# Kernel optimization log

Measured on AMD Instinct MI355X. Metric: run time of the kernel, lower is better.

Reference implementation:

```python
import jax, jax.numpy as jnp
import numpy as np

B, C, H, W = 64, 3, 64, 64
F = 96          # base_filters
K = 8           # n_mixtures
h, w = H // 2, W // 2
C0 = 2 * C      # channels of each checkerboard half
SECTIONS = [C0, C0, C0 * K, C0 * K, C0 * K]
SPLITS = [int(s) for s in np.cumsum(SECTIONS)[:-1]]
EPS = 1e-6


def conv2d(x, wgt, b):
    y = jax.lax.conv_general_dilated(x, wgt, (1, 1), 'SAME',
                                     dimension_numbers=('NCHW', 'OIHW', 'NCHW'))
    return y + b[None, :, None, None]


def layer_norm(x, g, b, eps=1e-5):
    # nn.LayerNorm(mid_shape): normalize over (C,H,W) per sample
    mu = jnp.mean(x, axis=(1, 2, 3), keepdims=True)
    var = jnp.var(x, axis=(1, 2, 3), keepdims=True)
    return (x - mu) / jnp.sqrt(var + eps) * g[None] + b[None]


def checker_split(z, odd=False):
    Bz, Cz, Hz, Wz = z.shape
    z = z.reshape(Bz, Cz, Hz // 2, 2, Wz // 2, 2)
    p00 = z[:, :, :, 0, :, 0]; p01 = z[:, :, :, 0, :, 1]
    p10 = z[:, :, :, 1, :, 0]; p11 = z[:, :, :, 1, :, 1]
    z0 = jnp.concatenate([p00, p11], axis=1)  # even checkerboard
    z1 = jnp.concatenate([p01, p10], axis=1)  # odd checkerboard
    if odd:
        z0, z1 = z1, z0
    return z0, z1


def checker_merge(z0, z1, odd=False):
    if odd:
        z0, z1 = z1, z0
    Cz = z0.shape[1] // 2
    p00, p11 = z0[:, :Cz], z0[:, Cz:]
    p01, p10 = z1[:, :Cz], z1[:, Cz:]
    Bz, _, hz, wz = p00.shape
    zi = jnp.stack([jnp.stack([p00, p01], axis=-1),
                    jnp.stack([p10, p11], axis=-1)], axis=-2)  # (B,C,h,w,2i,2j)
    z = zi.transpose(0, 1, 2, 4, 3, 5).reshape(Bz, Cz, 2 * hz, 2 * wz)
    return z


def gated_attn(x, qkv_w, qkv_b, proj_w, proj_b):
    Bx, Fx, hx, wx = x.shape
    xf = x.reshape(Bx, Fx, hx * wx).transpose(0, 2, 1)  # (B, L, F)
    qkv = xf @ qkv_w.T + qkv_b
    q, k, v = jnp.split(qkv, 3, axis=-1)
    scores = jnp.einsum('bqf,bkf->bqk', q, k) / jnp.sqrt(jnp.float32(Fx))
    attn = jax.nn.softmax(scores, axis=-1)
    o = jnp.einsum('bqk,bkf->bqf', attn, v)
    g = o @ proj_w.T + proj_b
    ga, gb = jnp.split(g, 2, axis=-1)
    out = xf + ga * jax.nn.sigmoid(gb)  # gated residual
    return out.transpose(0, 2, 1).reshape(Bx, Fx, hx, wx)


def conditioner(z1, conv1_w, conv1_b, gconv_w, gconv_b, ln1_g, ln1_b,
                qkv_w, qkv_b, proj_w, proj_b, ln2_g, ln2_b, conv2_w, conv2_b):
    x = conv2d(z1, conv1_w, conv1_b)
    g = conv2d(x, gconv_w, gconv_b)
    ga, gb = jnp.split(g, 2, axis=1)
    x = x + ga * jax.nn.sigmoid(gb)          # GatedConv2d
    x = layer_norm(x, ln1_g, ln1_b)
    x = gated_attn(x, qkv_w, qkv_b, proj_w, proj_b)
    x = layer_norm(x, ln2_g, ln2_b)
    return conv2d(x, conv2_w, conv2_b)


def _forward(z, log_df_dz, conv1_w, conv1_b, gconv_w, gconv_b, ln1_g, ln1_b,
             qkv_w, qkv_b, proj_w, proj_b, ln2_g, ln2_b, conv2_w, conv2_b,
             a_log_scale, a_bias):
    z0, z1 = checker_split(z)
    params = conditioner(z1, conv1_w, conv1_b, gconv_w, gconv_b, ln1_g, ln1_b,
                         qkv_w, qkv_b, proj_w, proj_b, ln2_g, ln2_b, conv2_w, conv2_b)
    a, b, logpi, mu, s = jnp.split(params, SPLITS, axis=1)
    a = jnp.tanh(a) * a_log_scale + a_bias
    Bz = z0.shape[0]
    logpi = jax.nn.log_softmax(logpi.reshape(Bz, K, C0, h, w), axis=1)
    mu = mu.reshape(Bz, K, C0, h, w)
    s = s.reshape(Bz, K, C0, h, w)
    # mixture-of-logistics CDF
    u = (z0[:, None] - mu) * jnp.exp(-s)
    x = jnp.sum(jnp.exp(logpi) * jax.nn.sigmoid(u), axis=1)
    log_pdf = jax.scipy.special.logsumexp(
        logpi - s + jax.nn.log_sigmoid(u) + jax.nn.log_sigmoid(-u), axis=1)
    log_df_dz = log_df_dz + jnp.sum(log_pdf.reshape(Bz, -1), axis=1)
    # logit transform
    x = jnp.clip(x, EPS, 1.0 - EPS)
    z0n = jnp.log(x) - jnp.log1p(-x)
    log_df_dz = log_df_dz + jnp.sum((-jnp.log(x) - jnp.log1p(-x)).reshape(Bz, -1), axis=1)
    # affine rescale
    z0n = z0n * jnp.exp(a) + b
    log_df_dz = log_df_dz + jnp.sum(a.reshape(Bz, -1), axis=1)
    return checker_merge(z0n, z1), log_df_dz


def setup_inputs() -> dict:
    key = jax.random.key(0)
    ks = jax.random.split(key, 10)
    sc = 0.05
    return dict(
        z=jax.random.normal(ks[0], (B, C, H, W), jnp.float32),
        log_df_dz=jnp.zeros((B,), jnp.float32),
        conv1_w=sc * jax.random.normal(ks[1], (F, C0, 3, 3), jnp.float32),
        conv1_b=jnp.zeros((F,), jnp.float32),
        gconv_w=sc * jax.random.normal(ks[2], (2 * F, F, 3, 3), jnp.float32),
        gconv_b=jnp.zeros((2 * F,), jnp.float32),
        ln1_g=jnp.ones((F, h, w), jnp.float32),
        ln1_b=jnp.zeros((F, h, w), jnp.float32),
        qkv_w=sc * jax.random.normal(ks[3], (3 * F, F), jnp.float32),
        qkv_b=jnp.zeros((3 * F,), jnp.float32),
        proj_w=sc * jax.random.normal(ks[4], (2 * F, F), jnp.float32),
        proj_b=jnp.zeros((2 * F,), jnp.float32),
        ln2_g=jnp.ones((F, h, w), jnp.float32),
        ln2_b=jnp.zeros((F, h, w), jnp.float32),
        conv2_w=sc * jax.random.normal(ks[5], (sum(SECTIONS), F, 3, 3), jnp.float32),
        conv2_b=jnp.zeros((sum(SECTIONS),), jnp.float32),
        a_log_scale=0.01 * jax.random.normal(ks[6], (1,), jnp.float32),
        a_bias=0.01 * jax.random.normal(ks[7], (1,), jnp.float32),
    )


def reference(z, log_df_dz, conv1_w, conv1_b, gconv_w, gconv_b, ln1_g, ln1_b,
              qkv_w, qkv_b, proj_w, proj_b, ln2_g, ln2_b, conv2_w, conv2_b,
              a_log_scale, a_bias):
    return _forward(z, log_df_dz, conv1_w, conv1_b, gconv_w, gconv_b, ln1_g, ln1_b,
                    qkv_w, qkv_b, proj_w, proj_b, ln2_g, ln2_b, conv2_w, conv2_b,
                    a_log_scale, a_bias)
```

## Files before the change

### kernel.cpp

```cpp
#include <hip/hip_runtime.h>
#include <cstdint>
#include <cstddef>


typedef unsigned short u16;
typedef __attribute__((ext_vector_type(8))) short short8;
typedef __attribute__((ext_vector_type(4))) float f32x4;
typedef __attribute__((ext_vector_type(4))) unsigned int u32x4;

__device__ __forceinline__ float sigm(float x){ return 1.0f/(1.0f+__expf(-x)); }

__device__ __forceinline__ u16 f2bf(float f){
    unsigned int u = __float_as_uint(f);
    u += 0x7fffu + ((u >> 16) & 1u);
    return (u16)(u >> 16);
}
__device__ __forceinline__ float bf2f(u16 v){
    unsigned int u = ((unsigned int)v) << 16;
    return __uint_as_float(u);
}

__device__ __forceinline__ void dma16(const u16* g, u16* l){
    __builtin_amdgcn_global_load_lds(
        (const __attribute__((address_space(1))) void*)g,
        (__attribute__((address_space(3))) void*)l,
        16, 0, 0);
}

__device__ __forceinline__ float ex2(float x){
    float r; asm("v_exp_f32 %0, %1" : "=v"(r) : "v"(x)); return r;
}
__device__ __forceinline__ unsigned cvtpk(float lo, float hi){
    unsigned r; asm("v_cvt_pk_bf16_f32 %0, %1, %2" : "=v"(r) : "v"(lo), "v"(hi)); return r;
}
__device__ __forceinline__ void plswap32(unsigned &a, unsigned &b){
    asm("v_permlane32_swap_b32 %0, %1" : "+v"(a), "+v"(b));
}
__device__ __forceinline__ void plswap16(unsigned &a, unsigned &b){
    asm("v_permlane16_swap_b32 %0, %1" : "+v"(a), "+v"(b));
}

#define SOFTPACK(S, LACC, PA) do { \
    unsigned pk_[4][2]; \
    _Pragma("unroll") \
    for (int t=0;t<4;++t){ \
        float e0 = ex2(S[t][0]); \
        float e1 = ex2(S[t][1]); \
        float e2 = ex2(S[t][2]); \
        float e3 = ex2(S[t][3]); \
        LACC += (e0+e1)+(e2+e3); \
        pk_[t][0] = cvtpk(e0,e1); \
        pk_[t][1] = cvtpk(e2,e3); \
    } \
    _Pragma("unroll") \
    for (int kk=0;kk<2;++kk){ \
        unsigned a0 = pk_[2*kk][0], b0 = pk_[2*kk+1][0]; \
        unsigned a1 = pk_[2*kk][1], b1 = pk_[2*kk+1][1]; \
        plswap32(a0,b0); plswap16(a0,b0); \
        plswap32(a1,b1); plswap16(a1,b1); \
        u32x4 dw_; dw_[0]=a0; dw_[1]=a1; dw_[2]=b0; dw_[3]=b1; \
        PA[kk] = __builtin_bit_cast(short8, dw_); \
    } \
} while(0)

__device__ __forceinline__ short8 ln_frag(const u16* __restrict__ xg,
    const float* __restrict__ gt, const float* __restrict__ bt,
    int p, int c0, float mu, float rr)
{
    short8 x8 = *reinterpret_cast<const short8*>(xg + (size_t)p*96 + c0);
    const float* gp = gt + (size_t)p*96 + c0;
    const float* bp = bt + (size_t)p*96 + c0;
    short8 o;
    #pragma unroll
    for (int j=0;j<8;++j){
        float ag = rr*gp[j];
        o[j] = (short)f2bf(bf2f((u16)x8[j])*ag + (bp[j] - mu*ag));
    }
    return o;
}

__global__ __launch_bounds__(256) void k_prep(
    const float* __restrict__ z, const float* __restrict__ c1w, const float* __restrict__ c1b,
    const float* __restrict__ gw, const float* __restrict__ c2w,
    const float* __restrict__ qkvw, const float* __restrict__ pw,
    const float* __restrict__ ln1g, const float* __restrict__ ln1b,
    const float* __restrict__ ln2g, const float* __restrict__ ln2b,
    const float* __restrict__ logdf,
    u16* __restrict__ x1b,
    u16* __restrict__ Wg, u16* __restrict__ W2,
    u16* __restrict__ Wqkv, u16* __restrict__ Wproj,
    float* __restrict__ gt1, float* __restrict__ bt1,
    float* __restrict__ gt2, float* __restrict__ bt2,
    float* __restrict__ outlog)
{
    int blk = blockIdx.x;
    int tid = threadIdx.x;
    __shared__ float tin[6][6][34];
    __shared__ __align__(16) u16 Wc[96][72];
    __shared__ __align__(16) u16 imc[128][72];

    if (blk < 512){
        int b  = blk >> 3;
        int pg = blk & 7;
        int r0 = pg*4;
        for (int e = tid; e < 96*72; e += 256){
            int oc = e/72, k = e%72;
            Wc[oc][k] = (k < 54) ? f2bf(c1w[oc*54 + k]) : (u16)0;
        }
        for (int idx = tid; idx < 6*6*34; idx += 256){
            int c = idx/204, rem = idx%204;
            int rr = rem/34, q = rem%34;
            int ii = r0 - 1 + rr, jj = q - 1;
            float v = 0.f;
            if ((unsigned)ii < 32u && (unsigned)jj < 32u){
                if (c < 3) v = z[((b*3+c)*64 + 2*ii)*64 + (2*jj+1)];
                else       v = z[((b*3+(c-3))*64 + (2*ii+1))*64 + 2*jj];
            }
            tin[c][rr][q] = v;
        }
        __syncthreads();
        for (int e = tid; e < 128*72; e += 256){
            int px = e/72, k = e%72;
            float v = 0.f;
            if (k < 54){
                int c = k/9, rr = (k%9)/3, dcc = k%3;
                v = tin[c][(px>>5)+rr][(px&31)+dcc];
            }
            imc[px][k] = f2bf(v);
        }
        __syncthreads();

        int w = tid >> 6, lane = tid & 63;
        int cc = lane & 15, gg = lane >> 4;
        f32x4 acc[2][6];
        #pragma unroll
        for (int u=0;u<2;++u)
            #pragma unroll
            for (int t=0;t<6;++t) acc[u][t] = (f32x4){0.f,0.f,0.f,0.f};

        #pragma unroll
        for (int ks=0; ks<2; ++ks){
            short8 a0 = *reinterpret_cast<const short8*>(&imc[w*32 + cc     ][ks*32 + 8*gg]);
            short8 a1 = *reinterpret_cast<const short8*>(&imc[w*32 + 16 + cc][ks*32 + 8*gg]);
            #pragma unroll
            for (int t=0; t<6; ++t){
                short8 bb = *reinterpret_cast<const short8*>(&Wc[t*16+cc][ks*32 + 8*gg]);
                acc[0][t] = __builtin_amdgcn_mfma_f32_16x16x32_bf16(a0, bb, acc[0][t], 0,0,0);
                acc[1][t] = __builtin_amdgcn_mfma_f32_16x16x32_bf16(a1, bb, acc[1][t], 0,0,0);
            }
        }

        #pragma unroll
        for (int u=0;u<2;++u){
            int p0 = pg*128 + w*32 + u*16 + gg*4;
            #pragma unroll
            for (int t=0;t<6;++t){
                int oc = t*16+cc;
                float bv = c1b[oc];
                #pragma unroll
                for (int r=0;r<4;++r)
                    x1b[((size_t)(b*1024) + p0 + r)*96 + oc] = f2bf(acc[u][t][r] + bv);
            }
        }
    } else if (blk < 1160){
        int idx = (blk-512)*256 + tid;
        int j = idx & 7;
        int lane = (idx >> 3) & 63;
        int fo = idx >> 9;
        int frag = fo % 18;
        int tob = fo / 18;
        int obk = tob & 1, tap = tob >> 1;
        int t = frag/3, ks = frag%3;
        int cc = lane & 15, gg = lane >> 4;
        int ocp = obk*96 + t*16 + cc;
        int r2 = ocp%96, isB = r2/48, i2 = r2%48;
        int oc = (ocp/96)*48 + i2 + isB*96;
        int ic = ks*32 + 8*gg + j;
        Wg[idx] = f2bf(gw[(size_t)(oc*96+ic)*9 + tap]);
    } else if (blk < 1700){
        int idx = (blk-1160)*256 + tid;
        int j = idx & 7;
        int lane = (idx >> 3) & 63;
        int fo = idx >> 9;
        int frag = fo % 15;
        int tob = fo / 15;
        int obk = tob & 1, tap = tob >> 1;
        int t = frag/3, ks = frag%3;
        int cc = lane & 15, gg = lane >> 4;
        int oc = obk*80 + t*16 + cc;
        int ic = ks*32 + 8*gg + j;
        W2[idx] = (oc < 156) ? f2bf(c2w[(size_t)(oc*96+ic)*9 + tap]) : (u16)0;
    } else if (blk < 1808){
        int idx = (blk-1700)*256 + tid;
        int j = idx & 7;
        int lane = (idx >> 3) & 63;
        int fo = idx >> 9;
        int frag = fo % 27;
        int obk = fo / 27;
        int t = frag/3, ks = frag%3;
        int cc = lane & 15, gg = lane >> 4;
        int n = obk*144 + t*16 + cc;
        int ic = ks*32 + 8*gg + j;
        Wqkv[idx] = f2bf(qkvw[(size_t)n*96 + ic]);
    } else if (blk < 1880){
        int idx = (blk-1808)*256 + tid;
        int j = idx & 7;
        int lane = (idx >> 3) & 63;
        int fo = idx >> 9;
        int frag = fo % 18;
        int obk = fo / 18;
        int t = frag/3, ks = frag%3;
        int cc = lane & 15, gg = lane >> 4;
        int ocp = obk*96 + t*16 + cc;
        int r2 = ocp%96, isB = r2/48, i2 = r2%48;
        int oc = obk*48 + i2 + isB*96;
        int ic = ks*32 + 8*gg + j;
        Wproj[idx] = f2bf(pw[(size_t)oc*96 + ic]);
    } else if (blk < 2264){
        int idx = (blk-1880)*256 + tid;
        int c = idx >> 10, p = idx & 1023;
        gt1[p*96 + c] = ln1g[idx];
    } else if (blk < 2648){
        int idx = (blk-2264)*256 + tid;
        int c = idx >> 10, p = idx & 1023;
        bt1[p*96 + c] = ln1b[idx];
    } else if (blk < 3032){
        int idx = (blk-2648)*256 + tid;
        int c = idx >> 10, p = idx & 1023;
        gt2[p*96 + c] = ln2g[idx];
    } else if (blk < 3416){
        int idx = (blk-3032)*256 + tid;
        int c = idx >> 10, p = idx & 1023;
        bt2[p*96 + c] = ln2b[idx];
    } else {
        if (tid < 64) outlog[tid] = logdf[tid];
    }
}

__global__ __launch_bounds__(256,4) void k_gconv(const u16* __restrict__ Xpb,
    const u16* __restrict__ Wt, const float* __restrict__ bias,
    u16* __restrict__ outb, float* __restrict__ partials)
{
    int blk  = blockIdx.x;
    int obk  = blk & 1;
    int pblk = (blk >> 1) & 7;
    int b    = blk >> 4;
    int tid  = threadIdx.x;
    int w = tid >> 6, lane = tid & 63;
    int cc = lane & 15, gg = lane >> 4;

    __shared__ __align__(16) u16 Ws[2][9216];
    __shared__ float red[8];

    f32x4 acc[2][6];
    #pragma unroll
    for (int u=0;u<2;++u)
        #pragma unroll
        for (int t=0;t<6;++t) acc[u][t] = (f32x4){0.f,0.f,0.f,0.f};

    int base = pblk*128 + w*32;
    int ia = base >> 5;
    const u16* xb = Xpb + (size_t)b*1024*96;

    {
        const u16* src = Wt + (size_t)obk*9216;
        #pragma unroll
        for (int i=0;i<5;++i){
            int c = tid + 256*i;
            if (c < 1152) dma16(src + (size_t)c*8, Ws[0] + (size_t)(w*64+256*i)*8);
        }
    }

    for (int tap=0; tap<9; ++tap){
        __syncthreads();
        if (tap < 8){
            const u16* src = Wt + (size_t)((tap+1)*2 + obk)*9216;
            int nb = (tap+1)&1;
            #pragma unroll
            for (int i=0;i<5;++i){
                int c = tid + 256*i;
                if (c < 1152) dma16(src + (size_t)c*8, Ws[nb] + (size_t)(w*64+256*i)*8);
            }
        }
        const u16* Wc = Ws[tap&1];
        int dr = tap/3 - 1, dc = tap%3 - 1;

        int ii = ia + dr;
        int jj0 = cc + dc, jj1 = cc + 16 + dc;
        bool rv = ((unsigned)ii < 32u);
        bool v0 = rv && ((unsigned)jj0 < 32u);
        bool v1 = rv && ((unsigned)jj1 < 32u);
        const u16* ar0 = xb + (ptrdiff_t)(ii*32 + jj0)*96 + 8*gg;
        const u16* ar1 = xb + (ptrdiff_t)(ii*32 + jj1)*96 + 8*gg;

        #pragma unroll
        for (int ks=0; ks<3; ++ks){
            short8 a0 = {0,0,0,0,0,0,0,0};
            short8 a1 = {0,0,0,0,0,0,0,0};
            if (v0) a0 = *reinterpret_cast<const short8*>(ar0 + ks*32);
            if (v1) a1 = *reinterpret_cast<const short8*>(ar1 + ks*32);
            #pragma unroll
            for (int t=0; t<6; ++t){
                short8 bb = *reinterpret_cast<const short8*>(Wc + ((size_t)(t*3+ks)*64 + lane)*8);
                acc[0][t] = __builtin_amdgcn_mfma_f32_16x16x32_bf16(a0, bb, acc[0][t], 0,0,0);
                acc[1][t] = __builtin_amdgcn_mfma_f32_16x16x32_bf16(a1, bb, acc[1][t], 0,0,0);
            }
        }
    }

    float s = 0.f, ssq = 0.f;
    #pragma unroll
    for (int u=0;u<2;++u){
        int p0 = base + u*16 + gg*4;
        #pragma unroll
        for (int t=0;t<3;++t){
            int ocA = obk*48 + t*16+cc;
            float ba = bias[ocA], bbv = bias[ocA+96];
            #pragma unroll
            for (int r=0;r<4;++r){
                float res = bf2f(Xpb[((size_t)b*1024 + p0+r)*96 + ocA]);
                float va = acc[u][t][r]   + ba;
                float vb = acc[u][t+3][r] + bbv;
                float v = res + va*sigm(vb);
                outb[((size_t)b*1024 + p0+r)*96 + ocA] = f2bf(v);
                s += v; ssq += v*v;
            }
        }
    }
    #pragma unroll
    for (int o=32;o>0;o>>=1){ s += __shfl_down(s,o,64); ssq += __shfl_down(ssq,o,64); }
    if (lane==0){ red[w]=s; red[4+w]=ssq; }
    __syncthreads();
    if (tid==0){
        int slot = b*16 + pblk*2 + obk;
        partials[slot*2+0] = red[0]+red[1]+red[2]+red[3];
        partials[slot*2+1] = red[4]+red[5]+red[6]+red[7];
    }
}

__global__ __launch_bounds__(256) void k_lne(const u16* __restrict__ xb,
    const float* __restrict__ gt, const float* __restrict__ bt,
    const float* __restrict__ partials, u16* __restrict__ out)
{
    int b = blockIdx.x / 48, rem = blockIdx.x % 48;
    float s=0.f, ss=0.f;
    #pragma unroll
    for (int i=0;i<16;++i){ s += partials[(b*16+i)*2]; ss += partials[(b*16+i)*2+1]; }
    float mu = s/98304.f;
    float r = rsqrtf(ss/98304.f - mu*mu + 1e-5f);

    int e8 = rem*256 + threadIdx.x;
    size_t base = (size_t)b*98304 + (size_t)e8*8;
    short8 x8 = *reinterpret_cast<const short8*>(xb + base);
    const float* gp = gt + e8*8;
    const float* bp = bt + e8*8;
    short8 o8;
    #pragma unroll
    for (int i=0;i<8;++i)
        o8[i] = (short)f2bf((bf2f((u16)x8[i]) - mu)*r*gp[i] + bp[i]);
    *reinterpret_cast<short8*>(out + base) = o8;
}

__global__ __launch_bounds__(256,4) void k_qkvm(const u16* __restrict__ Xg,
    const float* __restrict__ gt, const float* __restrict__ bt,
    const float* __restrict__ part,
    const u16* __restrict__ Wt, const float* __restrict__ bias,
    u16* __restrict__ Qb, u16* __restrict__ Kf, u16* __restrict__ Vf)
{
    int blk  = blockIdx.x;
    int obk  = blk & 1;
    int pblk = (blk >> 1) & 7;
    int b    = blk >> 4;
    int tid  = threadIdx.x;
    int w = tid >> 6, lane = tid & 63;
    int cc = lane & 15, gg = lane >> 4;
    const float scale = 0.14724445f;

    __shared__ __align__(16) u16 Ws[13824];
    {
        const u16* src = Wt + (size_t)obk*13824;
        #pragma unroll
        for (int i=0;i<7;++i){
            int c = tid + 256*i;
            if (c < 1728) dma16(src + (size_t)c*8, Ws + (size_t)(w*64+256*i)*8);
        }
    }

    float sS=0.f, sQ=0.f;
    #pragma unroll
    for (int i=0;i<16;++i){ sS += part[(b*16+i)*2]; sQ += part[(b*16+i)*2+1]; }
    float mu = sS/98304.f;
    float rr = rsqrtf(sQ/98304.f - mu*mu + 1e-5f);

    f32x4 acc[2][9];
    #pragma unroll
    for (int u=0;u<2;++u)
        #pragma unroll
        for (int t=0;t<9;++t) acc[u][t] = (f32x4){0.f,0.f,0.f,0.f};

    int base = pblk*128 + w*32;
    const u16* xg = Xg + (size_t)b*1024*96;
    __syncthreads();

    #pragma unroll
    for (int ks=0; ks<3; ++ks){
        int c0 = ks*32 + 8*gg;
        short8 a0 = ln_frag(xg, gt, bt, base+cc,    c0, mu, rr);
        short8 a1 = ln_frag(xg, gt, bt, base+cc+16, c0, mu, rr);
        #pragma unroll
        for (int t=0; t<9; ++t){
            short8 bb = *reinterpret_cast<const short8*>(Ws + ((size_t)(t*3+ks)*64 + lane)*8);
            acc[0][t] = __builtin_amdgcn_mfma_f32_16x16x32_bf16(a0, bb, acc[0][t], 0,0,0);
            acc[1][t] = __builtin_amdgcn_mfma_f32_16x16x32_bf16(a1, bb, acc[1][t], 0,0,0);
        }
    }

    #pragma unroll
    for (int u=0;u<2;++u){
        int p0 = base + u*16 + gg*4;
        #pragma unroll
        for (int t=0;t<9;++t){
            int n = obk*144 + t*16+cc;
            float bv = bias[n];
            #pragma unroll
            for (int r=0;r<4;++r){
                int p = p0 + r;
                float av = acc[u][t][r] + bv;
                if (n < 96){
                    Qb[((size_t)(b*1024+p))*96 + n] = f2bf(av*scale);
                } else if (n < 192){
                    int f = n-96;
                    int jt = p>>6, t16 = (p>>4)&3, ccs = p&15;
                    int ks = f>>5, ggs = (f>>3)&3, j = f&7;
                    Kf[(size_t)(b*16+jt)*6144 + (size_t)(((t16*3+ks)*4+ggs)*16+ccs)*8 + j] = f2bf(av);
                } else {
                    int f = n-192;
                    int jt = p>>6, kl = p&63;
                    int kk = kl>>5, ggs = (kl>>3)&3, j = kl&7;
                    int ft = f>>4, ccs = f&15;
                    Vf[(size_t)(b*16+jt)*6144 + (size_t)(((ft*2+kk)*4+ggs)*16+ccs)*8 + j] = f2bf(av);
                }
            }
        }
    }
}

__global__ __launch_bounds__(256,2) void k_attnproj(const u16* __restrict__ Qb,
    const u16* __restrict__ Kf, const u16* __restrict__ Vf,
    const u16* __restrict__ Wpg, const float* __restrict__ pbias,
    const u16* __restrict__ Xg, const float* __restrict__ gt, const float* __restrict__ bt,
    const float* __restrict__ part1,
    u16* __restrict__ outb, float* __restrict__ partials)
{
    int qt = blockIdx.x >> 6;
    int b  = blockIdx.x & 63;
    int tid = threadIdx.x;
    int w  = tid >> 6;
    int lane = tid & 63;
    int cc = lane & 15;
    int gg = lane >> 4;

    __shared__ __align__(16) u16 SM[36864];
    __shared__ float red[16];

    u16* Ksb = SM;
    u16* Vsb = SM + 18432;
    u16* Wp  = SM;
    u16* Ot  = SM + 18432;

    float sS=0.f, sQ=0.f;
    #pragma unroll
    for (int i=0;i<16;++i){ sS += part1[(b*16+i)*2]; sQ += part1[(b*16+i)*2+1]; }
    float mu1 = sS/98304.f;
    float rr1 = rsqrtf(sQ/98304.f - mu1*mu1 + 1e-5f);

    int q0 = qt*128 + w*32;

    short8 qf[2][3];
    {
        const u16* qr0 = Qb + ((size_t)(b*1024 + q0 + cc))*96;
        #pragma unroll
        for (int ks=0; ks<3; ++ks){
            qf[0][ks] = *reinterpret_cast<const short8*>(qr0 + ks*32 + 8*gg);
            qf[1][ks] = *reinterpret_cast<const short8*>(qr0 + (size_t)16*96 + ks*32 + 8*gg);
        }
    }

    f32x4 Oacc[2][6];
    #pragma unroll
    for (int u=0;u<2;++u)
        #pragma unroll
        for (int ft=0; ft<6; ++ft) Oacc[u][ft] = (f32x4){0.f,0.f,0.f,0.f};
    float l_acc[2] = {0.f, 0.f};

    const u16* Kb0 = Kf + (size_t)(b*16)*6144;
    const u16* Vb0 = Vf + (size_t)(b*16)*6144;

    #pragma unroll
    for (int i=0;i<3;++i){
        size_t c8 = (size_t)(tid + 256*i)*8;
        size_t l8 = (size_t)(w*64 + 256*i)*8;
        dma16(Kb0 + c8, Ksb + l8);
        dma16(Vb0 + c8, Vsb + l8);
    }
    #pragma unroll
    for (int i=0;i<3;++i){
        size_t c8 = (size_t)(6144 + (tid + 256*i)*8);
        size_t l8 = (size_t)(w*64 + 256*i)*8;
        dma16(Kb0 + c8, Ksb + 6144 + l8);
        dma16(Vb0 + c8, Vsb + 6144 + l8);
    }

    for (int jt=0; jt<16; ++jt){
        if (jt < 15) asm volatile("s_waitcnt vmcnt(6)" ::: "memory");
        else         asm volatile("s_waitcnt vmcnt(0)" ::: "memory");
        __builtin_amdgcn_s_barrier();
        __builtin_amdgcn_sched_barrier(0);

        if (jt < 14){
            const u16* kn = Kb0 + (size_t)(jt+2)*6144;
            const u16* vn = Vb0 + (size_t)(jt+2)*6144;
            u16* kd = Ksb + (size_t)((jt+2)%3)*6144;
            u16* vd = Vsb + (size_t)((jt+2)%3)*6144;
            #pragma unroll
            for (int i=0;i<3;++i){
                size_t c8 = (size_t)(tid + 256*i)*8;
                size_t l8 = (size_t)(w*64 + 256*i)*8;
                dma16(kn + c8, kd + l8);
                dma16(vn + c8, vd + l8);
            }
        }

        const u16* Kc = Ksb + (size_t)(jt%3)*6144;
        const u16* Vc = Vsb + (size_t)(jt%3)*6144;

        f32x4 S0[4], S1[4];
        #pragma unroll
        for (int t=0;t<4;++t){ S0[t] = (f32x4){0.f,0.f,0.f,0.f}; S1[t] = (f32x4){0.f,0.f,0.f,0.f}; }

        __builtin_amdgcn_s_setprio(1);
        #pragma unroll
        for (int ks=0; ks<3; ++ks){
            #pragma unroll
            for (int t=0; t<4; ++t){
                short8 kb = *reinterpret_cast<const short8*>(Kc + ((t*3+ks)*64 + lane)*8);
                S0[t] = __builtin_amdgcn_mfma_f32_16x16x32_bf16(kb, qf[0][ks], S0[t], 0,0,0);
                S1[t] = __builtin_amdgcn_mfma_f32_16x16x32_bf16(kb, qf[1][ks], S1[t], 0,0,0);
            }
        }
        __builtin_amdgcn_s_setprio(0);

        short8 pa0[2], pa1[2];
        SOFTPACK(S0, l_acc[0], pa0);
        SOFTPACK(S1, l_acc[1], pa1);

        __builtin_amdgcn_s_setprio(1);
        #pragma unroll
        for (int kk=0; kk<2; ++kk){
            #pragma unroll
            for (int ft=0; ft<6; ++ft){
                short8 vb = *reinterpret_cast<const short8*>(Vc + ((ft*2+kk)*64 + lane)*8);
                Oacc[0][ft] = __builtin_amdgcn_mfma_f32_16x16x32_bf16(pa0[kk], vb, Oacc[0][ft], 0,0,0);
                Oacc[1][ft] = __builtin_amdgcn_mfma_f32_16x16x32_bf16(pa1[kk], vb, Oacc[1][ft], 0,0,0);
            }
        }
        __builtin_amdgcn_s_setprio(0);
    }

    __syncthreads();

    #pragma unroll
    for (int i=0;i<9;++i){
        int c = tid + 256*i;
        dma16(Wpg + (size_t)c*8, Wp + (size_t)(w*64+256*i)*8);
    }

    #pragma unroll
    for (int u=0;u<2;++u){
        float lv = l_acc[u];
        lv += __shfl_xor(lv, 16, 64);
        lv += __shfl_xor(lv, 32, 64);
        float linv[4];
        #pragma unroll
        for (int r=0;r<4;++r) linv[r] = 1.0f / __shfl(lv, 4*gg + r, 64);
        #pragma unroll
        for (int ft=0; ft<6; ++ft)
            #pragma unroll
            for (int r=0; r<4; ++r)
                Ot[(size_t)(w*32 + u*16 + 4*gg + r)*104 + ft*16 + cc]
                    = f2bf(Oacc[u][ft][r]*linv[r]);
    }

    __syncthreads();

    f32x4 pacc[2][12];
    #pragma unroll
    for (int u=0;u<2;++u)
        #pragma unroll
        for (int t=0;t<12;++t) pacc[u][t] = (f32x4){0.f,0.f,0.f,0.f};

    #pragma unroll
    for (int ks=0; ks<3; ++ks){
        short8 a0 = *reinterpret_cast<const short8*>(Ot + (size_t)(w*32 + cc     )*104 + ks*32 + 8*gg);
        short8 a1 = *reinterpret_cast<const short8*>(Ot + (size_t)(w*32 + cc + 16)*104 + ks*32 + 8*gg);
        #pragma unroll
        for (int t2=0; t2<12; ++t2){
            int obk = t2/6, tl = t2%6;
            short8 bb = *reinterpret_cast<const short8*>(Wp + ((size_t)(obk*18 + tl*3 + ks)*64 + lane)*8);
            pacc[0][t2] = __builtin_amdgcn_mfma_f32_16x16x32_bf16(a0, bb, pacc[0][t2], 0,0,0);
            pacc[1][t2] = __builtin_amdgcn_mfma_f32_16x16x32_bf16(a1, bb, pacc[1][t2], 0,0,0);
        }
    }

    const u16* resb = Xg + (size_t)b*1024*96;
    float s0=0.f, q0s=0.f, s1=0.f, q1s=0.f;
    #pragma unroll
    for (int u=0;u<2;++u){
        int p0 = qt*128 + w*32 + u*16 + gg*4;
        #pragma unroll
        for (int obk=0;obk<2;++obk){
            #pragma unroll
            for (int tl=0;tl<3;++tl){
                int ocA = obk*48 + tl*16 + cc;
                float ba = pbias[ocA], bbv = pbias[ocA+96];
                #pragma unroll
                for (int r=0;r<4;++r){
                    int pl = p0 + r;
                    float ga = pacc[u][obk*6+tl][r]   + ba;
                    float gb = pacc[u][obk*6+tl+3][r] + bbv;
                    float xv = bf2f(resb[(size_t)pl*96 + ocA]);
                    float res = (xv - mu1)*rr1*gt[(size_t)pl*96 + ocA] + bt[(size_t)pl*96 + ocA];
                    float v = res + ga * sigm(gb);
                    outb[((size_t)b*1024 + pl)*96 + ocA] = f2bf(v);
                    if (obk==0){ s0 += v; q0s += v*v; } else { s1 += v; q1s += v*v; }
                }
            }
        }
    }
    #pragma unroll
    for (int o=32;o>0;o>>=1){
        s0 += __shfl_down(s0,o,64);  q0s += __shfl_down(q0s,o,64);
        s1 += __shfl_down(s1,o,64);  q1s += __shfl_down(q1s,o,64);
    }
    if (lane==0){ red[w*4+0]=s0; red[w*4+1]=q0s; red[w*4+2]=s1; red[w*4+3]=q1s; }
    __syncthreads();
    if (tid==0){
        int slot = b*16 + qt*2;
        partials[(size_t)slot*2+0]     = red[0]+red[4]+red[8]+red[12];
        partials[(size_t)slot*2+1]     = red[1]+red[5]+red[9]+red[13];
        partials[(size_t)(slot+1)*2+0] = red[2]+red[6]+red[10]+red[14];
        partials[(size_t)(slot+1)*2+1] = red[3]+red[7]+red[11]+red[15];
    }
}

__global__ __launch_bounds__(256,2) void k_c2mix(const u16* __restrict__ Xpb,
    const u16* __restrict__ Wt, const float* __restrict__ bias,
    const float* __restrict__ z, const float* __restrict__ a_ls_p,
    const float* __restrict__ a_b_p, float* __restrict__ out_z, float* __restrict__ out_log)
{
    int blk  = blockIdx.x;
    int pblk = blk & 7;
    int b    = blk >> 3;
    int tid  = threadIdx.x;
    int w = tid >> 6, lane = tid & 63;
    int cc = lane & 15, gg = lane >> 4;

    __shared__ __align__(16) u16 SM[30720];
    __shared__ float red[4];

    f32x4 acc[2][10];
    #pragma unroll
    for (int u=0;u<2;++u)
        #pragma unroll
        for (int t=0;t<10;++t) acc[u][t] = (f32x4){0.f,0.f,0.f,0.f};

    int base = pblk*128 + w*32;
    int ia = base >> 5;
    const u16* xb = Xpb + (size_t)b*1024*96;

    {
        #pragma unroll
        for (int i=0;i<8;++i){
            int c = tid + 256*i;
            if (c < 1920) dma16(Wt + (size_t)c*8, SM + (size_t)(w*64+256*i)*8);
        }
    }

    for (int tap=0; tap<9; ++tap){
        __syncthreads();
        if (tap < 8){
            const u16* src = Wt + (size_t)(tap+1)*15360;
            u16* dst = SM + (size_t)((tap+1)&1)*15360;
            #pragma unroll
            for (int i=0;i<8;++i){
                int c = tid + 256*i;
                if (c < 1920) dma16(src + (size_t)c*8, dst + (size_t)(w*64+256*i)*8);
            }
        }
        const u16* Wc = SM + (size_t)(tap&1)*15360;
        int dr = tap/3 - 1, dc = tap%3 - 1;

        int ii = ia + dr;
        int jj0 = cc + dc, jj1 = cc + 16 + dc;
        bool rv = ((unsigned)ii < 32u);
        bool v0 = rv && ((unsigned)jj0 < 32u);
        bool v1 = rv && ((unsigned)jj1 < 32u);
        const u16* ar0 = xb + (ptrdiff_t)(ii*32 + jj0)*96 + 8*gg;
        const u16* ar1 = xb + (ptrdiff_t)(ii*32 + jj1)*96 + 8*gg;

        #pragma unroll
        for (int ks=0; ks<3; ++ks){
            short8 a0 = {0,0,0,0,0,0,0,0};
            short8 a1 = {0,0,0,0,0,0,0,0};
            if (v0) a0 = *reinterpret_cast<const short8*>(ar0 + ks*32);
            if (v1) a1 = *reinterpret_cast<const short8*>(ar1 + ks*32);
            #pragma unroll
            for (int t=0; t<10; ++t){
                int fl = (t<5) ? (t*3+ks) : (15 + (t-5)*3 + ks);
                short8 bb = *reinterpret_cast<const short8*>(Wc + ((size_t)fl*64 + lane)*8);
                acc[0][t] = __builtin_amdgcn_mfma_f32_16x16x32_bf16(a0, bb, acc[0][t], 0,0,0);
                acc[1][t] = __builtin_amdgcn_mfma_f32_16x16x32_bf16(a1, bb, acc[1][t], 0,0,0);
            }
        }
    }

    __syncthreads();
    #pragma unroll
    for (int u=0;u<2;++u){
        int lp0 = w*32 + u*16 + gg*4;
        #pragma unroll
        for (int t=0;t<10;++t){
            int oc = (t<5) ? (t*16+cc) : (80 + (t-5)*16 + cc);
            if (oc < 156){
                float bv = bias[oc];
                #pragma unroll
                for (int r=0;r<4;++r)
                    SM[oc*132 + lp0 + r] = f2bf(acc[u][t][r] + bv);
            }
        }
    }
    __syncthreads();

    float als = a_ls_p[0], abv = a_b_p[0];
    float logsum = 0.f;
    #pragma unroll
    for (int e3=0;e3<3;++e3){
        int e  = tid + 256*e3;
        int c0 = e >> 7, xp = e & 127;
        int pix = pblk*128 + xp;
        int i = pix >> 5, j = pix & 31;

        if (c0 < 3){
            int idx01 = ((b*3+c0)*64 + 2*i)*64 + 2*j+1;
            int idx10 = ((b*3+c0)*64 + 2*i+1)*64 + 2*j;
            out_z[idx01] = z[idx01];
            out_z[idx10] = z[idx10];
        }

        float z0v = (c0<3) ? z[((b*3+c0)*64 + 2*i)*64 + 2*j]
                           : z[((b*3+(c0-3))*64 + 2*i+1)*64 + 2*j+1];
        float a_raw = bf2f(SM[(c0)*132 + xp]);
        float bco   = bf2f(SM[(6+c0)*132 + xp]);
        float lpk[8], muk[8], svk[8];
        float m1 = -1e30f;
        #pragma unroll
        for (int k=0;k<8;++k){
            lpk[k] = bf2f(SM[(12 + k*6 + c0)*132 + xp]);
            muk[k] = bf2f(SM[(60 + k*6 + c0)*132 + xp]);
            svk[k] = bf2f(SM[(108 + k*6 + c0)*132 + xp]);
            m1 = fmaxf(m1, lpk[k]);
        }
        float se = 0.f;
        #pragma unroll
        for (int k=0;k<8;++k) se += __expf(lpk[k]-m1);
        float lse = m1 + __logf(se);
        float xm = 0.f, mt = -1e30f;
        float tk[8];
        #pragma unroll
        for (int k=0;k<8;++k){
            float lpn = lpk[k] - lse;
            float u = (z0v - muk[k]) * __expf(-svk[k]);
            float au = fabsf(u);
            xm += __expf(lpn) * (1.f/(1.f+__expf(-u)));
            float lss = -(au + 2.f*log1pf(__expf(-au)));
            float t2 = lpn - svk[k] + lss;
            tk[k] = t2; mt = fmaxf(mt, t2);
        }
        float se2 = 0.f;
        #pragma unroll
        for (int k=0;k<8;++k) se2 += __expf(tk[k]-mt);
        float logacc = mt + __logf(se2);
        xm = fminf(fmaxf(xm, 1e-6f), 1.f-1e-6f);
        float lx = __logf(xm), l1x = log1pf(-xm);
        logacc += -lx - l1x;
        float aa = tanhf(a_raw)*als + abv;
        float z0n = (lx - l1x)*__expf(aa) + bco;
        logacc += aa;
        int oidx = (c0<3) ? ((b*3+c0)*64 + 2*i)*64 + 2*j
                          : ((b*3+(c0-3))*64 + 2*i+1)*64 + 2*j+1;
        out_z[oidx] = z0n;
        logsum += logacc;
    }

    #pragma unroll
    for (int o=32;o>0;o>>=1) logsum += __shfl_down(logsum, o, 64);
    if (lane==0) red[w] = logsum;
    __syncthreads();
    if (tid==0) atomicAdd(out_log + b, red[0]+red[1]+red[2]+red[3]);
}

extern "C" void kernel_launch(void* const* d_in, const int* in_sizes, int n_in,
                              void* d_out, int out_size, void* d_ws, size_t ws_size,
                              hipStream_t stream)
{
    const float* z     = (const float*)d_in[0];
    const float* logdf = (const float*)d_in[1];
    const float* c1w   = (const float*)d_in[2];
    const float* c1b   = (const float*)d_in[3];
    const float* gw    = (const float*)d_in[4];
    const float* gcb   = (const float*)d_in[5];
    const float* ln1g  = (const float*)d_in[6];
    const float* ln1b  = (const float*)d_in[7];
    const float* qkvw  = (const float*)d_in[8];
    const float* qkvb  = (const float*)d_in[9];
    const float* pw    = (const float*)d_in[10];
    const float* pbb   = (const float*)d_in[11];
    const float* ln2g  = (const float*)d_in[12];
    const float* ln2b  = (const float*)d_in[13];
    const float* c2w   = (const float*)d_in[14];
    const float* c2b   = (const float*)d_in[15];
    const float* als   = (const float*)d_in[16];
    const float* ab    = (const float*)d_in[17];

    float* out_z   = (float*)d_out;
    float* out_log = out_z + 786432;

    float* ws     = (float*)d_ws;
    u16*   x1b    = (u16*)(ws + 0);
    u16*   xg_b   = (u16*)(ws + 3145728);
    u16*   Kf     = (u16*)(ws + 6291456);
    u16*   Vf     = (u16*)(ws + 9437184);
    u16*   x2b    = (u16*)(ws + 15728640);
    u16*   Qb     = x1b;
    u16*   xln2b  = Kf;
    const size_t T = 19660800;
    float* gt1    = ws + T;
    float* bt1    = ws + T + 98304;
    float* gt2    = ws + T + 196608;
    float* bt2    = ws + T + 294912;
    float* part1  = ws + T + 393216;
    float* part2  = ws + T + 395264;
    u16*   Wg     = (u16*)(ws + T + 397568);
    u16*   W2     = (u16*)(ws + T + 480512);
    u16*   Wqkv   = (u16*)(ws + T + 549632);
    u16*   Wproj  = (u16*)(ws + T + 563456);

    k_prep     <<<3417, 256, 0, stream>>>(z, c1w, c1b, gw, c2w, qkvw, pw,
                                          ln1g, ln1b, ln2g, ln2b, logdf,
                                          x1b, Wg, W2, Wqkv, Wproj,
                                          gt1, bt1, gt2, bt2, out_log);
    k_gconv    <<<1024, 256, 0, stream>>>(x1b, Wg, gcb, xg_b, part1);
    k_qkvm     <<<1024, 256, 0, stream>>>(xg_b, gt1, bt1, part1, Wqkv, qkvb, Qb, Kf, Vf);
    k_attnproj <<<512,  256, 0, stream>>>(Qb, Kf, Vf, Wproj, pbb,
                                          xg_b, gt1, bt1, part1, x2b, part2);
    k_lne      <<<3072, 256, 0, stream>>>(x2b, gt2, bt2, part2, xln2b);
    k_c2mix    <<<512,  256, 0, stream>>>(xln2b, W2, c2b, z, als, ab, out_z, out_log);
}
```

Before: 247.0 us.

## Fuse second LayerNorm into conv2 kernel and stage conv inputs in LDS

```diff
diff --git a/kernel.cpp b/kernel.cpp
--- a/kernel.cpp
+++ b/kernel.cpp
@@ -237,7 +237,7 @@
     }
 }
 
-__global__ __launch_bounds__(256,4) void k_gconv(const u16* __restrict__ Xpb,
+__global__ __launch_bounds__(256,2) void k_gconv(const u16* __restrict__ Xpb,
     const u16* __restrict__ Wt, const float* __restrict__ bias,
     u16* __restrict__ outb, float* __restrict__ partials)
 {
@@ -249,19 +249,27 @@
     int w = tid >> 6, lane = tid & 63;
     int cc = lane & 15, gg = lane >> 4;
 
+    __shared__ __align__(16) u16 As[18432];
     __shared__ __align__(16) u16 Ws[2][9216];
     __shared__ float red[8];
 
-    f32x4 acc[2][6];
-    #pragma unroll
-    for (int u=0;u<2;++u)
-        #pragma unroll
-        for (int t=0;t<6;++t) acc[u][t] = (f32x4){0.f,0.f,0.f,0.f};
-
-    int base = pblk*128 + w*32;
-    int ia = base >> 5;
     const u16* xb = Xpb + (size_t)b*1024*96;
 
+    {
+        int rowbase = pblk*4 - 1;
+        #pragma unroll
+        for (int i=0;i<9;++i){
+            int e = tid + 256*i;
+            int px = e/12, sub = e%12;
+            int ks = sub >> 2, g2 = sub & 3;
+            int lr = px >> 5, col = px & 31;
+            int grow = rowbase + lr;
+            short8 v = {0,0,0,0,0,0,0,0};
+            if ((unsigned)grow < 32u)
+                v = *reinterpret_cast<const short8*>(xb + (size_t)(grow*32+col)*96 + ks*32 + 8*g2);
+            *reinterpret_cast<short8*>(As + ((size_t)((lr*3+ks)*4+g2)*32 + col)*8) = v;
+        }
+    }
     {
         const u16* src = Wt + (size_t)obk*9216;
         #pragma unroll
@@ -270,6 +278,14 @@
             if (c < 1152) dma16(src + (size_t)c*8, Ws[0] + (size_t)(w*64+256*i)*8);
         }
     }
+
+    f32x4 acc[2][6];
+    #pragma unroll
+    for (int u=0;u<2;++u)
+        #pragma unroll
+        for (int t=0;t<6;++t) acc[u][t] = (f32x4){0.f,0.f,0.f,0.f};
+
+    int base = pblk*128 + w*32;
 
     for (int tap=0; tap<9; ++tap){
         __syncthreads();
@@ -285,20 +301,18 @@
         const u16* Wc = Ws[tap&1];
         int dr = tap/3 - 1, dc = tap%3 - 1;
 
-        int ii = ia + dr;
+        int lrr = w + 1 + dr;
         int jj0 = cc + dc, jj1 = cc + 16 + dc;
-        bool rv = ((unsigned)ii < 32u);
-        bool v0 = rv && ((unsigned)jj0 < 32u);
-        bool v1 = rv && ((unsigned)jj1 < 32u);
-        const u16* ar0 = xb + (ptrdiff_t)(ii*32 + jj0)*96 + 8*gg;
-        const u16* ar1 = xb + (ptrdiff_t)(ii*32 + jj1)*96 + 8*gg;
+        bool v0 = ((unsigned)jj0 < 32u);
+        bool v1 = ((unsigned)jj1 < 32u);
 
         #pragma unroll
         for (int ks=0; ks<3; ++ks){
+            const u16* ab = As + ((size_t)((lrr*3+ks)*4 + gg)*32)*8;
             short8 a0 = {0,0,0,0,0,0,0,0};
             short8 a1 = {0,0,0,0,0,0,0,0};
-            if (v0) a0 = *reinterpret_cast<const short8*>(ar0 + ks*32);
-            if (v1) a1 = *reinterpret_cast<const short8*>(ar1 + ks*32);
+            if (v0) a0 = *reinterpret_cast<const short8*>(ab + jj0*8);
+            if (v1) a1 = *reinterpret_cast<const short8*>(ab + jj1*8);
             #pragma unroll
             for (int t=0; t<6; ++t){
                 short8 bb = *reinterpret_cast<const short8*>(Wc + ((size_t)(t*3+ks)*64 + lane)*8);
@@ -336,29 +350,6 @@
         partials[slot*2+0] = red[0]+red[1]+red[2]+red[3];
         partials[slot*2+1] = red[4]+red[5]+red[6]+red[7];
     }
-}
-
-__global__ __launch_bounds__(256) void k_lne(const u16* __restrict__ xb,
-    const float* __restrict__ gt, const float* __restrict__ bt,
-    const float* __restrict__ partials, u16* __restrict__ out)
-{
-    int b = blockIdx.x / 48, rem = blockIdx.x % 48;
-    float s=0.f, ss=0.f;
-    #pragma unroll
-    for (int i=0;i<16;++i){ s += partials[(b*16+i)*2]; ss += partials[(b*16+i)*2+1]; }
-    float mu = s/98304.f;
-    float r = rsqrtf(ss/98304.f - mu*mu + 1e-5f);
-
-    int e8 = rem*256 + threadIdx.x;
-    size_t base = (size_t)b*98304 + (size_t)e8*8;
-    short8 x8 = *reinterpret_cast<const short8*>(xb + base);
-    const float* gp = gt + e8*8;
-    const float* bp = bt + e8*8;
-    short8 o8;
-    #pragma unroll
-    for (int i=0;i<8;++i)
-        o8[i] = (short)f2bf((bf2f((u16)x8[i]) - mu)*r*gp[i] + bp[i]);
-    *reinterpret_cast<short8*>(out + base) = o8;
 }
 
 __global__ __launch_bounds__(256,4) void k_qkvm(const u16* __restrict__ Xg,
@@ -653,7 +644,9 @@
     }
 }
 
-__global__ __launch_bounds__(256,2) void k_c2mix(const u16* __restrict__ Xpb,
+__global__ __launch_bounds__(256,2) void k_c2mix(const u16* __restrict__ X2,
+    const float* __restrict__ gt, const float* __restrict__ bt,
+    const float* __restrict__ part2,
     const u16* __restrict__ Wt, const float* __restrict__ bias,
     const float* __restrict__ z, const float* __restrict__ a_ls_p,
     const float* __restrict__ a_b_p, float* __restrict__ out_z, float* __restrict__ out_log)
@@ -665,66 +658,93 @@
     int w = tid >> 6, lane = tid & 63;
     int cc = lane & 15, gg = lane >> 4;
 
-    __shared__ __align__(16) u16 SM[30720];
+    __shared__ __align__(16) u16 SM[33792];
     __shared__ float red[4];
-
-    f32x4 acc[2][10];
-    #pragma unroll
-    for (int u=0;u<2;++u)
-        #pragma unroll
-        for (int t=0;t<10;++t) acc[u][t] = (f32x4){0.f,0.f,0.f,0.f};
-
-    int base = pblk*128 + w*32;
-    int ia = base >> 5;
-    const u16* xb = Xpb + (size_t)b*1024*96;
-
+    u16* As   = SM;
+    u16* Wbuf = SM + 18432;
+
+    float sS=0.f, sQ=0.f;
+    #pragma unroll
+    for (int i=0;i<16;++i){ sS += part2[(b*16+i)*2]; sQ += part2[(b*16+i)*2+1]; }
+    float mu2 = sS/98304.f;
+    float rr2 = rsqrtf(sQ/98304.f - mu2*mu2 + 1e-5f);
+
+    const u16* xb2 = X2 + (size_t)b*1024*96;
+
+    {
+        int rowbase = pblk*4 - 1;
+        #pragma unroll
+        for (int i=0;i<9;++i){
+            int e = tid + 256*i;
+            int px = e/12, sub = e%12;
+            int ks = sub >> 2, g2 = sub & 3;
+            int lr = px >> 5, col = px & 31;
+            int grow = rowbase + lr;
+            short8 v = {0,0,0,0,0,0,0,0};
+            if ((unsigned)grow < 32u){
+                size_t gp = (size_t)(grow*32+col)*96 + ks*32 + 8*g2;
+                short8 x8 = *reinterpret_cast<const short8*>(xb2 + gp);
+                const float* gpp = gt + gp;
+                const float* bpp = bt + gp;
+                #pragma unroll
+                for (int j=0;j<8;++j){
+                    float ag = rr2*gpp[j];
+                    v[j] = (short)f2bf(bf2f((u16)x8[j])*ag + (bpp[j] - mu2*ag));
+                }
+            }
+            *reinterpret_cast<short8*>(As + ((size_t)((lr*3+ks)*4+g2)*32 + col)*8) = v;
+        }
+    }
     {
         #pragma unroll
         for (int i=0;i<8;++i){
             int c = tid + 256*i;
-            if (c < 1920) dma16(Wt + (size_t)c*8, SM + (size_t)(w*64+256*i)*8);
-        }
-    }
+            if (c < 1920) dma16(Wt + (size_t)c*8, Wbuf + (size_t)(w*64+256*i)*8);
+        }
+    }
+
+    f32x4 acc[2][10];
+    #pragma unroll
+    for (int u=0;u<2;++u)
+        #pragma unroll
+        for (int t=0;t<10;++t) acc[u][t] = (f32x4){0.f,0.f,0.f,0.f};
 
     for (int tap=0; tap<9; ++tap){
+        __syncthreads();
+        int dr = tap/3 - 1, dc = tap%3 - 1;
+
+        int lrr = w + 1 + dr;
+        int jj0 = cc + dc, jj1 = cc + 16 + dc;
+        bool v0 = ((unsigned)jj0 < 32u);
+        bool v1 = ((unsigned)jj1 < 32u);
+
+        #pragma unroll
+        for (int ks=0; ks<3; ++ks){
+            const u16* ab = As + ((size_t)((lrr*3+ks)*4 + gg)*32)*8;
+            short8 a0 = {0,0,0,0,0,0,0,0};
+            short8 a1 = {0,0,0,0,0,0,0,0};
+            if (v0) a0 = *reinterpret_cast<const short8*>(ab + jj0*8);
+            if (v1) a1 = *reinterpret_cast<const short8*>(ab + jj1*8);
+            #pragma unroll
+            for (int t=0; t<10; ++t){
+                int fl = (t<5) ? (t*3+ks) : (15 + (t-5)*3 + ks);
+                short8 bb = *reinterpret_cast<const short8*>(Wbuf + ((size_t)fl*64 + lane)*8);
+                acc[0][t] = __builtin_amdgcn_mfma_f32_16x16x32_bf16(a0, bb, acc[0][t], 0,0,0);
+                acc[1][t] = __builtin_amdgcn_mfma_f32_16x16x32_bf16(a1, bb, acc[1][t], 0,0,0);
+            }
+        }
+
         __syncthreads();
         if (tap < 8){
             const u16* src = Wt + (size_t)(tap+1)*15360;
-            u16* dst = SM + (size_t)((tap+1)&1)*15360;
             #pragma unroll
             for (int i=0;i<8;++i){
                 int c = tid + 256*i;
-                if (c < 1920) dma16(src + (size_t)c*8, dst + (size_t)(w*64+256*i)*8);
-            }
-        }
-        const u16* Wc = SM + (size_t)(tap&1)*15360;
-        int dr = tap/3 - 1, dc = tap%3 - 1;
-
-        int ii = ia + dr;
-        int jj0 = cc + dc, jj1 = cc + 16 + dc;
-        bool rv = ((unsigned)ii < 32u);
-        bool v0 = rv && ((unsigned)jj0 < 32u);
-        bool v1 = rv && ((unsigned)jj1 < 32u);
-        const u16* ar0 = xb + (ptrdiff_t)(ii*32 + jj0)*96 + 8*gg;
-        const u16* ar1 = xb + (ptrdiff_t)(ii*32 + jj1)*96 + 8*gg;
-
-        #pragma unroll
-        for (int ks=0; ks<3; ++ks){
-            short8 a0 = {0,0,0,0,0,0,0,0};
-            short8 a1 = {0,0,0,0,0,0,0,0};
-            if (v0) a0 = *reinterpret_cast<const short8*>(ar0 + ks*32);
-            if (v1) a1 = *reinterpret_cast<const short8*>(ar1 + ks*32);
-            #pragma unroll
-            for (int t=0; t<10; ++t){
-                int fl = (t<5) ? (t*3+ks) : (15 + (t-5)*3 + ks);
-                short8 bb = *reinterpret_cast<const short8*>(Wc + ((size_t)fl*64 + lane)*8);
-                acc[0][t] = __builtin_amdgcn_mfma_f32_16x16x32_bf16(a0, bb, acc[0][t], 0,0,0);
-                acc[1][t] = __builtin_amdgcn_mfma_f32_16x16x32_bf16(a1, bb, acc[1][t], 0,0,0);
-            }
-        }
-    }
-
-    __syncthreads();
+                if (c < 1920) dma16(src + (size_t)c*8, Wbuf + (size_t)(w*64+256*i)*8);
+            }
+        }
+    }
+
     #pragma unroll
     for (int u=0;u<2;++u){
         int lp0 = w*32 + u*16 + gg*4;
@@ -842,7 +862,6 @@
     u16*   Vf     = (u16*)(ws + 9437184);
     u16*   x2b    = (u16*)(ws + 15728640);
     u16*   Qb     = x1b;
-    u16*   xln2b  = Kf;
     const size_t T = 19660800;
     float* gt1    = ws + T;
     float* bt1    = ws + T + 98304;
@@ -863,6 +882,6 @@
     k_qkvm     <<<1024, 256, 0, stream>>>(xg_b, gt1, bt1, part1, Wqkv, qkvb, Qb, Kf, Vf);
     k_attnproj <<<512,  256, 0, stream>>>(Qb, Kf, Vf, Wproj, pbb,
                                           xg_b, gt1, bt1, part1, x2b, part2);
-    k_lne      <<<3072, 256, 0, stream>>>(x2b, gt2, bt2, part2, xln2b);
-    k_c2mix    <<<512,  256, 0, stream>>>(xln2b, W2, c2b, z, als, ab, out_z, out_log);
-}
+    k_c2mix    <<<512,  256, 0, stream>>>(x2b, gt2, bt2, part2, W2, c2b, z, als, ab,
+                                          out_z, out_log);
+}
```

Measured after the change: 316.2 us. 1.28x slower.

## Stage K/V epilogue through LDS and write fragments with coalesced 16-byte stores

Applied to the files above, without the earlier changes.

```diff
diff --git a/kernel.cpp b/kernel.cpp
--- a/kernel.cpp
+++ b/kernel.cpp
@@ -199,7 +199,9 @@
         int obk = fo / 27;
         int t = frag/3, ks = frag%3;
         int cc = lane & 15, gg = lane >> 4;
-        int n = obk*144 + t*16 + cc;
+        int n;
+        if (obk==0) n = (t<6) ? (t*16+cc)      : (192 + (t-6)*16 + cc);
+        else        n = (t<6) ? (96 + t*16+cc) : (240 + (t-6)*16 + cc);
         int ic = ks*32 + 8*gg + j;
         Wqkv[idx] = f2bf(qkvw[(size_t)n*96 + ic]);
     } else if (blk < 1880){
@@ -376,7 +378,8 @@
     int cc = lane & 15, gg = lane >> 4;
     const float scale = 0.14724445f;
 
-    __shared__ __align__(16) u16 Ws[13824];
+    __shared__ __align__(16) u16 SM[18432];
+    u16* Ws = SM;
     {
         const u16* src = Wt + (size_t)obk*13824;
         #pragma unroll
@@ -415,32 +418,85 @@
         }
     }
 
-    #pragma unroll
-    for (int u=0;u<2;++u){
-        int p0 = base + u*16 + gg*4;
-        #pragma unroll
-        for (int t=0;t<9;++t){
-            int n = obk*144 + t*16+cc;
-            float bv = bias[n];
-            #pragma unroll
-            for (int r=0;r<4;++r){
-                int p = p0 + r;
-                float av = acc[u][t][r] + bv;
-                if (n < 96){
-                    Qb[((size_t)(b*1024+p))*96 + n] = f2bf(av*scale);
-                } else if (n < 192){
-                    int f = n-96;
-                    int jt = p>>6, t16 = (p>>4)&3, ccs = p&15;
-                    int ks = f>>5, ggs = (f>>3)&3, j = f&7;
-                    Kf[(size_t)(b*16+jt)*6144 + (size_t)(((t16*3+ks)*4+ggs)*16+ccs)*8 + j] = f2bf(av);
-                } else {
-                    int f = n-192;
-                    int jt = p>>6, kl = p&63;
-                    int kk = kl>>5, ggs = (kl>>3)&3, j = kl&7;
-                    int ft = f>>4, ccs = f&15;
-                    Vf[(size_t)(b*16+jt)*6144 + (size_t)(((ft*2+kk)*4+ggs)*16+ccs)*8 + j] = f2bf(av);
+    __syncthreads();
+
+    if (obk == 0){
+        #pragma unroll
+        for (int u=0;u<2;++u){
+            int p0 = base + u*16 + gg*4;
+            #pragma unroll
+            for (int t=0;t<9;++t){
+                #pragma unroll
+                for (int r=0;r<4;++r){
+                    int p = p0 + r;
+                    if (t < 6){
+                        int n = t*16+cc;
+                        float av = acc[u][t][r] + bias[n];
+                        Qb[((size_t)(b*1024+p))*96 + n] = f2bf(av*scale);
+                    } else {
+                        int f = (t-6)*16+cc;
+                        float av = acc[u][t][r] + bias[192+f];
+                        int jtl = (p>>6)&1;
+                        int kl = p&63;
+                        int kk=kl>>5, ggs=(kl>>3)&3, j=kl&7;
+                        int ft=f>>4, ccs=f&15;
+                        int slot = ((ft*2+kk)*4+ggs)*16+ccs;
+                        SM[jtl*3072 + slot*8 + j] = f2bf(av);
+                    }
                 }
             }
+        }
+        __syncthreads();
+        #pragma unroll
+        for (int i=0;i<3;++i){
+            int c = tid + 256*i;
+            int jtp = c/384, off = c%384;
+            *reinterpret_cast<short8*>(Vf + (size_t)(b*16 + pblk*2 + jtp)*6144 + (size_t)off*8)
+                = *reinterpret_cast<const short8*>(SM + (size_t)c*8);
+        }
+    } else {
+        #pragma unroll
+        for (int u=0;u<2;++u){
+            int p0 = base + u*16 + gg*4;
+            #pragma unroll
+            for (int t=0;t<9;++t){
+                #pragma unroll
+                for (int r=0;r<4;++r){
+                    int p = p0 + r;
+                    int jtl = (p>>6)&1;
+                    if (t < 6){
+                        int f = t*16+cc;
+                        float av = acc[u][t][r] + bias[96+f];
+                        int t16 = (p>>4)&3, ccs = p&15;
+                        int ks = f>>5, ggs=(f>>3)&3, j=f&7;
+                        int slot = ((t16*3+ks)*4+ggs)*16+ccs;
+                        SM[jtl*6144 + slot*8 + j] = f2bf(av);
+                    } else {
+                        int f = 48 + (t-6)*16+cc;
+                        float av = acc[u][t][r] + bias[192+f];
+                        int kl = p&63;
+                        int kk=kl>>5, ggs=(kl>>3)&3, j=kl&7;
+                        int ft=f>>4, ccs=f&15;
+                        int slot = ((ft*2+kk)*4+ggs)*16+ccs;
+                        SM[12288 + jtl*3072 + (slot-384)*8 + j] = f2bf(av);
+                    }
+                }
+            }
+        }
+        __syncthreads();
+        #pragma unroll
+        for (int i=0;i<6;++i){
+            int c = tid + 256*i;
+            int jtp = c/768, off = c%768;
+            *reinterpret_cast<short8*>(Kf + (size_t)(b*16 + pblk*2 + jtp)*6144 + (size_t)off*8)
+                = *reinterpret_cast<const short8*>(SM + (size_t)c*8);
+        }
+        #pragma unroll
+        for (int i=0;i<3;++i){
+            int c = tid + 256*i;
+            int jtp = c/384, off = c%384;
+            *reinterpret_cast<short8*>(Vf + (size_t)(b*16 + pblk*2 + jtp)*6144 + 3072 + (size_t)off*8)
+                = *reinterpret_cast<const short8*>(SM + 12288 + (size_t)c*8);
         }
     }
 }
```

Measured after the change: 292.1 us. 18.3% more time.
